# Kernel optimization log

Hardware: AMD Instinct MI355X
Metric: run time of the kernel (lower is better)

Reference implementation:

```python
import jax, jax.numpy as jnp
import numpy as np

# Dimensions (AlphaFold-scale IPA / GeometricFrameAttention)
B, N = 1, 768
C_S, C_Z, C_H, H, PQ, PV = 384, 128, 16, 12, 4, 8
INF = 1e9
EPS = 1e-8
SOFTPLUS_INV_1 = 0.541324854612918  # gfa_point_weights_init_


def quat_to_rot(q):
    """Unit-normalize quaternions [..., 4] -> rotation matrices [..., 3, 3]."""
    q = q / jnp.linalg.norm(q, axis=-1, keepdims=True)
    w, x, y, z = q[..., 0], q[..., 1], q[..., 2], q[..., 3]
    R = jnp.stack([
        1 - 2 * (y * y + z * z), 2 * (x * y - w * z), 2 * (x * z + w * y),
        2 * (x * y + w * z), 1 - 2 * (x * x + z * z), 2 * (y * z - w * x),
        2 * (x * z - w * y), 2 * (y * z + w * x), 1 - 2 * (x * x + y * y),
    ], axis=-1)
    return R.reshape(q.shape[:-1] + (3, 3))


def setup_inputs() -> dict:
    key = jax.random.key(0)
    ks = jax.random.split(key, 12)

    def lin(k, out_d, in_d):
        return jax.random.normal(k, (out_d, in_d), jnp.float32) * (1.0 / np.sqrt(in_d))

    out_in = H * C_H + H * PV * 4 + H * C_Z  # o + o_pt(x,y,z) + o_pt_norm + o_pair
    inp = {
        "s": jax.random.normal(ks[0], (B, N, C_S), jnp.float32),
        "z": jax.random.normal(ks[1], (B, N, N, C_Z), jnp.float32),
        "rot": quat_to_rot(jax.random.normal(ks[2], (B, N, 4), jnp.float32)),
        "trans": jax.random.normal(ks[3], (B, N, 3), jnp.float32),
        "mask": jnp.ones((B, N), jnp.float32),
        "Wq": lin(ks[4], H * C_H, C_S),
        "bq": jnp.zeros((H * C_H,), jnp.float32),
        "Wkv": lin(ks[5], H * 2 * C_H, C_S),
        "bkv": jnp.zeros((H * 2 * C_H,), jnp.float32),
        "Wqp": lin(ks[6], H * PQ * 3, C_S),
        "bqp": jnp.zeros((H * PQ * 3,), jnp.float32),
        "Wkvp": lin(ks[7], H * (PQ + PV) * 3, C_S),
        "bkvp": jnp.zeros((H * (PQ + PV) * 3,), jnp.float32),
        "Wb": lin(ks[8], H, C_Z),
        "bb": jnp.zeros((H,), jnp.float32),
        "head_w": jnp.full((H,), SOFTPLUS_INV_1, jnp.float32),
        "Wout": lin(ks[9], C_S, out_in),
        "bout": jnp.zeros((C_S,), jnp.float32),
    }
    return inp


def _forward(s, z, rot, trans, mask, Wq, bq, Wkv, bkv, Wqp, bqp, Wkvp, bkvp,
             Wb, bb, head_w, Wout, bout):
    Bn, Nn, _ = s.shape
    # scalar q/k/v
    q = (s @ Wq.T + bq).reshape(Bn, Nn, H, C_H)
    kv = (s @ Wkv.T + bkv).reshape(Bn, Nn, H, 2 * C_H)
    k, v = kv[..., :C_H], kv[..., C_H:]
    # point q/k/v: local frame -> global frame (x_glob = R x_loc + t)
    q_pts = (s @ Wqp.T + bqp).reshape(Bn, Nn, H * PQ, 3)
    q_pts = (jnp.einsum('bnxy,bnpy->bnpx', rot, q_pts) + trans[:, :, None]).reshape(Bn, Nn, H, PQ, 3)
    kv_pts = (s @ Wkvp.T + bkvp).reshape(Bn, Nn, H * (PQ + PV), 3)
    kv_pts = (jnp.einsum('bnxy,bnpy->bnpx', rot, kv_pts) + trans[:, :, None]).reshape(Bn, Nn, H, PQ + PV, 3)
    k_pts, v_pts = kv_pts[..., :PQ, :], kv_pts[..., PQ:, :]
    # pair bias [B,N,N,H] -> [B,H,N,N]
    bias = z @ Wb.T + bb
    a = jnp.einsum('bihc,bjhc->bhij', q, k) * np.float32(np.sqrt(1.0 / (3 * C_H)))
    a = a + np.float32(np.sqrt(1.0 / 3.0)) * jnp.transpose(bias, (0, 3, 1, 2))
    # point distance term: sum_p |q_p - k_p|^2 = |q|^2 + |k|^2 - 2 q.k (no [B,N,N,H,P,3] tensor)
    q2 = jnp.sum(q_pts ** 2, axis=(-1, -2))  # [B,N,H]
    k2 = jnp.sum(k_pts ** 2, axis=(-1, -2))
    qk = jnp.einsum('bihpc,bjhpc->bhij', q_pts, k_pts)
    d2 = q2.transpose(0, 2, 1)[..., :, None] + k2.transpose(0, 2, 1)[..., None, :] - 2.0 * qk
    hw = jax.nn.softplus(head_w) * np.float32(np.sqrt(2.0 / (27.0 * PQ)))  # sqrt(1/(3*(PQ*9/2)))
    a = a - 0.5 * hw[None, :, None, None] * d2
    # mask bias
    sq_mask = mask[..., :, None] * mask[..., None, :]
    a = a + (INF * (sq_mask - 1.0))[:, None]
    a = jax.nn.softmax(a, axis=-1)  # [B,H,N,N]
    # outputs
    o = jnp.einsum('bhij,bjhc->bihc', a, v).reshape(Bn, Nn, H * C_H)
    o_pt = jnp.einsum('bhij,bjhpc->bihpc', a, v_pts)  # global frame
    o_pt = jnp.einsum('bnyx,bnhpy->bnhpx', rot, o_pt - trans[:, :, None, None])  # back to local
    o_pt_norm = jnp.sqrt(jnp.sum(o_pt ** 2, axis=-1) + EPS).reshape(Bn, Nn, H * PV)
    o_pt_flat = jnp.moveaxis(o_pt, -1, -3).reshape(Bn, Nn, 3 * H * PV)  # coord-major like unbind+cat
    o_pair = jnp.einsum('bhij,bijc->bihc', a, z).reshape(Bn, Nn, H * C_Z)
    cat = jnp.concatenate([o, o_pt_flat, o_pt_norm, o_pair], axis=-1)
    return cat @ Wout.T + bout


def reference(s, z, rot, trans, mask, Wq, bq, Wkv, bkv, Wqp, bqp, Wkvp, bkvp,
              Wb, bb, head_w, Wout, bout):
    return _forward(s, z, rot, trans, mask, Wq, bq, Wkv, bkv, Wqp, bqp,
                    Wkvp, bkvp, Wb, bb, head_w, Wout, bout)
```

## Files before the change

### kernel.cpp

```cpp
#include <hip/hip_runtime.h>
#include <math.h>

#define NN 768
#define CS 384
#define CZ 128
#define CH 16
#define HH 12
#define PQ 4
#define PV 8
#define OUTIN 2112

#define SC_QK 0.14433756729740643f
#define SC_B  0.57735026918962576f
#define SC_HW 0.13608276348795434f
#define MSLACK 12.0f

__device__ __forceinline__ float dpp_add(float x, const int ctrl) {
    int yi;
    switch (ctrl) {
        case 0: yi = __builtin_amdgcn_update_dpp(0, __float_as_int(x), 0xB1,  0xf, 0xf, true); break;
        case 1: yi = __builtin_amdgcn_update_dpp(0, __float_as_int(x), 0x4E,  0xf, 0xf, true); break;
        case 2: yi = __builtin_amdgcn_update_dpp(0, __float_as_int(x), 0x141, 0xf, 0xf, true); break;
        default:yi = __builtin_amdgcn_update_dpp(0, __float_as_int(x), 0x140, 0xf, 0xf, true); break;
    }
    return x + __int_as_float(yi);
}
__device__ __forceinline__ float dpp_max(float x, const int ctrl) {
    int yi;
    switch (ctrl) {
        case 0: yi = __builtin_amdgcn_update_dpp(0, __float_as_int(x), 0xB1,  0xf, 0xf, true); break;
        case 1: yi = __builtin_amdgcn_update_dpp(0, __float_as_int(x), 0x4E,  0xf, 0xf, true); break;
        case 2: yi = __builtin_amdgcn_update_dpp(0, __float_as_int(x), 0x141, 0xf, 0xf, true); break;
        default:yi = __builtin_amdgcn_update_dpp(0, __float_as_int(x), 0x140, 0xf, 0xf, true); break;
    }
    return fmaxf(x, __int_as_float(yi));
}

__global__ __launch_bounds__(256) void kproj(
    const float* __restrict__ s,
    const float* __restrict__ Wq,  const float* __restrict__ bq,
    const float* __restrict__ Wkv, const float* __restrict__ bkv,
    const float* __restrict__ Wqp, const float* __restrict__ bqp,
    const float* __restrict__ Wkvp,const float* __restrict__ bkvp,
    float* __restrict__ q, float* __restrict__ kT, float* __restrict__ vall,
    float* __restrict__ qpr, float* __restrict__ kvpr)
{
    __shared__ float s_lds[8*384];
    int n0 = blockIdx.x * 8;
    int t = threadIdx.x;
    for (int idx = t; idx < 8*384; idx += 256)
        s_lds[idx] = s[(n0 + idx/384)*384 + (idx%384)];
    __syncthreads();

    int o = blockIdx.y * 128 + (t & 127);
    int ng = t >> 7;
    const float* wrow; float bias;
    if (o < 192)      { wrow = Wq   + o*384;       bias = bq[o]; }
    else if (o < 576) { wrow = Wkv  + (o-192)*384; bias = bkv[o-192]; }
    else if (o < 720) { wrow = Wqp  + (o-576)*384; bias = bqp[o-576]; }
    else              { wrow = Wkvp + (o-720)*384; bias = bkvp[o-720]; }

    float acc[4] = {bias, bias, bias, bias};
    const float4* wr4 = reinterpret_cast<const float4*>(wrow);
    for (int c4 = 0; c4 < 96; ++c4) {
        float4 w = wr4[c4];
        #pragma unroll
        for (int nn = 0; nn < 4; ++nn) {
            const float* sr = &s_lds[(ng*4+nn)*384 + c4*4];
            acc[nn] = fmaf(w.x, sr[0], acc[nn]);
            acc[nn] = fmaf(w.y, sr[1], acc[nn]);
            acc[nn] = fmaf(w.z, sr[2], acc[nn]);
            acc[nn] = fmaf(w.w, sr[3], acc[nn]);
        }
    }
    #pragma unroll
    for (int nn = 0; nn < 4; ++nn) {
        int n = n0 + ng*4 + nn;
        float v = acc[nn];
        if (o < 192)      q[n*192 + o] = v;
        else if (o < 576) {
            int oo = o - 192, h = oo >> 5, cc = oo & 31;
            if (cc < 16) kT[(h*NN + n)*16 + cc] = v;
            else         vall[(size_t)n*480 + h*40 + (cc-16)] = v;
        }
        else if (o < 720) qpr[n*144 + (o-576)] = v;
        else              kvpr[n*432 + (o-720)] = v;
    }
}

__global__ __launch_bounds__(192) void krot(
    const float* __restrict__ rot, const float* __restrict__ trans,
    const float* __restrict__ qpr, const float* __restrict__ kvpr,
    float* __restrict__ qp, float* __restrict__ kpT, float* __restrict__ vall)
{
    int n = blockIdx.x;
    __shared__ float R[9], T[3];
    int t = threadIdx.x;
    if (t < 9) R[t] = rot[n*9 + t];
    if (t < 3) T[t] = trans[n*3 + t];
    __syncthreads();

    const float* src = (t < 48) ? (qpr + n*144 + t*3) : (kvpr + n*432 + (t-48)*3);
    float x = src[0], y = src[1], z = src[2];
    float wx = R[0]*x + R[1]*y + R[2]*z + T[0];
    float wy = R[3]*x + R[4]*y + R[5]*z + T[1];
    float wz = R[6]*x + R[7]*y + R[8]*z + T[2];
    if (t < 48) {
        float* d = qp + n*144 + t*3;
        d[0]=wx; d[1]=wy; d[2]=wz;
    } else {
        int pi = t - 48, h = pi/12, pp = pi%12;
        if (pp < 4) {
            float* d = kpT + (h*NN+n)*12 + pp*3;
            d[0]=wx; d[1]=wy; d[2]=wz;
        } else {
            float* d = vall + (size_t)n*480 + h*40 + 16 + (pp-4)*3;
            d[0]=wx; d[1]=wy; d[2]=wz;
        }
    }
}

__global__ __launch_bounds__(256) void kqk(
    const float* __restrict__ kT, const float* __restrict__ kpT,
    const float* __restrict__ q, const float* __restrict__ qp,
    const float* __restrict__ mask, const float* __restrict__ head_w,
    const float* __restrict__ bb, float* __restrict__ lqd,
    float* __restrict__ mpart)
{
    const int j0 = blockIdx.x * 64;
    const int i0 = blockIdx.y * 32;
    __shared__ float ktl[64][17], kpl[64][13];
    __shared__ float ql[32][17],  qpl[32][13];
    __shared__ float mi_l[32], mj_l[64];
    __shared__ float mpl[32][12];
    const int t = threadIdx.x;
    if (t < 32) mi_l[t] = mask[i0 + t];
    if (t < 64) mj_l[t] = mask[j0 + t];

    const int jl = t & 63, wv = t >> 6;

    for (int h = 0; h < 12; ++h) {
        __syncthreads();
        for (int idx = t; idx < 1024; idx += 256)
            ktl[idx >> 4][idx & 15] = kT[(size_t)(h*NN + j0 + (idx >> 4))*16 + (idx & 15)];
        for (int idx = t; idx < 768; idx += 256) {
            int r = idx / 12, e = idx - r*12;
            kpl[r][e] = kpT[(size_t)(h*NN + j0 + r)*12 + e];
        }
        for (int idx = t; idx < 512; idx += 256)
            ql[idx >> 4][idx & 15] = q[(i0 + (idx >> 4))*192 + h*16 + (idx & 15)];
        for (int idx = t; idx < 384; idx += 256) {
            int r = idx / 12, e = idx - r*12;
            qpl[r][e] = qp[(i0 + r)*144 + h*12 + e];
        }
        __syncthreads();

        const float hwh = log1pf(expf(head_w[h])) * SC_HW;
        const float bbh = bb[h] * SC_B;
        const float mj = mj_l[jl];
        #pragma unroll
        for (int k = 0; k < 8; ++k) {
            const int il = wv*8 + k;
            float qk = 0.f;
            #pragma unroll
            for (int c = 0; c < 16; ++c) qk = fmaf(ktl[jl][c], ql[il][c], qk);
            float d2 = 0.f;
            #pragma unroll
            for (int e = 0; e < 12; ++e) { float d = qpl[il][e] - kpl[jl][e]; d2 = fmaf(d, d, d2); }
            float mt = 1e9f * (mi_l[il]*mj - 1.0f);
            float lg = fmaf(qk, SC_QK, fmaf(-0.5f*hwh, d2, bbh)) + mt;
            lqd[((size_t)(i0+il)*NN + j0 + jl)*12 + h] = lg;
            float m = lg;
            m = dpp_max(m, 0);
            m = dpp_max(m, 1);
            m = dpp_max(m, 2);
            m = dpp_max(m, 3);
            m = fmaxf(m, __shfl_xor(m, 16, 64));
            m = fmaxf(m, __shfl_xor(m, 32, 64));
            if (jl == 0) mpl[il][h] = m;
        }
    }
    __syncthreads();
    if (t < 384) {
        int il = t / 12, h = t - il*12;
        mpart[((size_t)h*NN + i0 + il)*12 + blockIdx.x] = mpl[il][h];
    }
}

__global__ __launch_bounds__(256) void kfuse(
    const float* __restrict__ z, const float* __restrict__ Wb,
    const float* __restrict__ lqd, const float* __restrict__ mpart,
    const float* __restrict__ vall,
    float* __restrict__ opart, float* __restrict__ vpart, float* __restrict__ ssum)
{
    __shared__ float  M_lds[12];
    __shared__ __align__(16) float p_lds[12][68];
    __shared__ __align__(16) float p_T[64][16];
    __shared__ float2 ofold[4][12][64];
    __shared__ float  sredL[16][6];

    const int i = blockIdx.x, jseg = blockIdx.y;
    const int t = threadIdx.x, w = t >> 6, l = t & 63;
    const int gid = t >> 4, cl = t & 15;
    const int hhalf = gid & 1, h0 = hhalf * 6, jofs = gid >> 1;

    if (t < 12) {
        const float4* mp = (const float4*)(mpart + ((size_t)t*NN + i)*12);
        float4 a = mp[0], b = mp[1], c = mp[2];
        float m = fmaxf(fmaxf(fmaxf(a.x,a.y), fmaxf(a.z,a.w)),
                 fmaxf(fmaxf(fmaxf(b.x,b.y), fmaxf(b.z,b.w)),
                       fmaxf(fmaxf(c.x,c.y), fmaxf(c.z,c.w))));
        M_lds[t] = m + MSLACK;
    }

    float4 wva[6], wvb[6];
    #pragma unroll
    for (int h = 0; h < 6; ++h) {
        const float4* wp = (const float4*)(Wb + (h0+h)*CZ + cl*8);
        wva[h] = wp[0]; wvb[h] = wp[1];
    }

    float2 oa[12];
    #pragma unroll
    for (int h = 0; h < 12; ++h) { oa[h].x = 0.f; oa[h].y = 0.f; }
    float2 vacc; vacc.x = 0.f; vacc.y = 0.f;
    const int vch = 2*t;
    const int vh  = (t < 240) ? (vch / 40) : 0;
    float s_acc = 0.f;

    __syncthreads();
    const float Mh = M_lds[h0 + (cl < 6 ? cl : 5)];
    const int jbase = jseg * 192;

    for (int tile = 0; tile < 3; ++tile) {
        const int jt = jbase + tile*64;

        {
            const float4* zq0 = (const float4*)(z + ((size_t)i*NN + jt + jofs)*CZ) + cl*2;
            float4 za = zq0[0], zb = zq0[1];
            for (int it = 0; it < 8; ++it) {
                float4 zaN = za, zbN = zb;
                if (it + 1 < 8) {
                    const float4* zq = (const float4*)(z + ((size_t)i*NN + jt + (it+1)*8 + jofs)*CZ) + cl*2;
                    zaN = zq[0]; zbN = zq[1];
                }
                const int j = jt + it*8 + jofs;
                float b0, b1, b2, b3, b4, b5;
                #define BDOT(BV, H)                                \
                    BV = za.x*wva[H].x;                            \
                    BV = fmaf(za.y, wva[H].y, BV);                 \
                    BV = fmaf(za.z, wva[H].z, BV);                 \
                    BV = fmaf(za.w, wva[H].w, BV);                 \
                    BV = fmaf(zb.x, wvb[H].x, BV);                 \
                    BV = fmaf(zb.y, wvb[H].y, BV);                 \
                    BV = fmaf(zb.z, wvb[H].z, BV);                 \
                    BV = fmaf(zb.w, wvb[H].w, BV);
                BDOT(b0, 0) BDOT(b1, 1) BDOT(b2, 2) BDOT(b3, 3) BDOT(b4, 4) BDOT(b5, 5)
                #undef BDOT
                #define BRED(BV)                                   \
                    BV = dpp_add(BV, 0);                           \
                    BV = dpp_add(BV, 1);                           \
                    BV = dpp_add(BV, 2);                           \
                    BV = dpp_add(BV, 3);
                BRED(b0) BRED(b1) BRED(b2) BRED(b3) BRED(b4) BRED(b5)
                #undef BRED
                float bsel = b0;
                bsel = (cl == 1) ? b1 : bsel;
                bsel = (cl == 2) ? b2 : bsel;
                bsel = (cl == 3) ? b3 : bsel;
                bsel = (cl == 4) ? b4 : bsel;
                bsel = (cl == 5) ? b5 : bsel;
                if (cl < 6) {
                    float g = fmaf(bsel, SC_B, lqd[((size_t)i*NN + j)*12 + h0 + cl]);
                    float p = __expf(g - Mh);
                    p_lds[h0 + cl][j - jt] = p;
                    p_T[j - jt][h0 + cl] = p;
                    s_acc += p;
                }
                za = zaN; zb = zbN;
            }
        }
        __syncthreads();

        {
            const float2* zr2 = (const float2*)(z + (size_t)i*NN*CZ) + l;
            #pragma unroll 4
            for (int jj = 0; jj < 16; ++jj) {
                const int jb = jj*4 + w;
                float2 zv = zr2[(size_t)(jt + jb)*64];
                float4 pA = *(const float4*)&p_T[jb][0];
                float4 pB = *(const float4*)&p_T[jb][4];
                float4 pC = *(const float4*)&p_T[jb][8];
                oa[0].x  = fmaf(pA.x, zv.x, oa[0].x);  oa[0].y  = fmaf(pA.x, zv.y, oa[0].y);
                oa[1].x  = fmaf(pA.y, zv.x, oa[1].x);  oa[1].y  = fmaf(pA.y, zv.y, oa[1].y);
                oa[2].x  = fmaf(pA.z, zv.x, oa[2].x);  oa[2].y  = fmaf(pA.z, zv.y, oa[2].y);
                oa[3].x  = fmaf(pA.w, zv.x, oa[3].x);  oa[3].y  = fmaf(pA.w, zv.y, oa[3].y);
                oa[4].x  = fmaf(pB.x, zv.x, oa[4].x);  oa[4].y  = fmaf(pB.x, zv.y, oa[4].y);
                oa[5].x  = fmaf(pB.y, zv.x, oa[5].x);  oa[5].y  = fmaf(pB.y, zv.y, oa[5].y);
                oa[6].x  = fmaf(pB.z, zv.x, oa[6].x);  oa[6].y  = fmaf(pB.z, zv.y, oa[6].y);
                oa[7].x  = fmaf(pB.w, zv.x, oa[7].x);  oa[7].y  = fmaf(pB.w, zv.y, oa[7].y);
                oa[8].x  = fmaf(pC.x, zv.x, oa[8].x);  oa[8].y  = fmaf(pC.x, zv.y, oa[8].y);
                oa[9].x  = fmaf(pC.y, zv.x, oa[9].x);  oa[9].y  = fmaf(pC.y, zv.y, oa[9].y);
                oa[10].x = fmaf(pC.z, zv.x, oa[10].x); oa[10].y = fmaf(pC.z, zv.y, oa[10].y);
                oa[11].x = fmaf(pC.w, zv.x, oa[11].x); oa[11].y = fmaf(pC.w, zv.y, oa[11].y);
            }
        }

        if (t < 240) {
            const float2* vr = (const float2*)(vall + (size_t)jt*480 + vch);
            #pragma unroll 4
            for (int q4 = 0; q4 < 16; ++q4) {
                float4 pv = *(const float4*)&p_lds[vh][q4*4];
                float2 v0 = vr[(size_t)(q4*4+0)*240];
                float2 v1 = vr[(size_t)(q4*4+1)*240];
                float2 v2 = vr[(size_t)(q4*4+2)*240];
                float2 v3 = vr[(size_t)(q4*4+3)*240];
                vacc.x = fmaf(pv.x, v0.x, vacc.x); vacc.y = fmaf(pv.x, v0.y, vacc.y);
                vacc.x = fmaf(pv.y, v1.x, vacc.x); vacc.y = fmaf(pv.y, v1.y, vacc.y);
                vacc.x = fmaf(pv.z, v2.x, vacc.x); vacc.y = fmaf(pv.z, v2.y, vacc.y);
                vacc.x = fmaf(pv.w, v3.x, vacc.x); vacc.y = fmaf(pv.w, v3.y, vacc.y);
            }
        }
        __syncthreads();
    }

    #pragma unroll
    for (int h = 0; h < 12; ++h) ofold[w][h][l] = oa[h];
    if (cl < 6) sredL[gid][cl] = s_acc;
    if (t < 240)
        *((float2*)(vpart + ((size_t)(jseg*NN + i))*480) + t) = vacc;
    __syncthreads();

    float2* opw = (float2*)(opart + ((size_t)(jseg*NN + i))*1536);
    #pragma unroll
    for (int k = 0; k < 3; ++k) {
        int slot = k*256 + t;
        int h = slot >> 6, c2 = slot & 63;
        float2 v0 = ofold[0][h][c2], v1 = ofold[1][h][c2];
        float2 v2 = ofold[2][h][c2], v3 = ofold[3][h][c2];
        float2 o;
        o.x = v0.x + v1.x + v2.x + v3.x;
        o.y = v0.y + v1.y + v2.y + v3.y;
        opw[slot] = o;
    }
    if (t < 12) {
        float sv = 0.f;
        #pragma unroll
        for (int k = 0; k < 8; ++k) sv += sredL[k*2 + (t/6)][t % 6];
        ssum[(size_t)(jseg*12 + t)*NN + i] = sv;
    }
}

__global__ __launch_bounds__(256) void kepi(
    const float* __restrict__ opart, const float* __restrict__ vpart,
    const float* __restrict__ ssum, const float* __restrict__ rot,
    const float* __restrict__ trans, float* __restrict__ cat)
{
    __shared__ float sinv[12];
    __shared__ float optl[12][24];
    __shared__ float R[9], T[3];
    const int i = blockIdx.x, t = threadIdx.x;
    if (t < 9) R[t] = rot[i*9 + t];
    if (t < 3) T[t] = trans[i*3 + t];
    if (t >= 16 && t < 28) {
        int h = t - 16;
        sinv[h] = 1.0f / (ssum[(size_t)h*NN + i] + ssum[(size_t)(12+h)*NN + i]
                        + ssum[(size_t)(24+h)*NN + i] + ssum[(size_t)(36+h)*NN + i]);
    }
    __syncthreads();

    float* crow = cat + (size_t)i*OUTIN;
    const float2* op0 = (const float2*)(opart + (size_t)i*1536);
    const float2* op1 = (const float2*)(opart + (size_t)(NN + i)*1536);
    const float2* op2 = (const float2*)(opart + (size_t)(2*NN + i)*1536);
    const float2* op3 = (const float2*)(opart + (size_t)(3*NN + i)*1536);
    #pragma unroll
    for (int k = 0; k < 3; ++k) {
        int slot = k*256 + t;
        int h = slot >> 6, c2 = slot & 63;
        float2 a = op0[slot], b = op1[slot], c = op2[slot], d = op3[slot];
        float sc = sinv[h];
        float2 o;
        o.x = (a.x + b.x + c.x + d.x)*sc;
        o.y = (a.y + b.y + c.y + d.y)*sc;
        *(float2*)(crow + 576 + h*128 + c2*2) = o;
    }
    if (t < 240) {
        const int ch = 2*t, h = ch/40, e = ch%40;
        float2 v0 = *(const float2*)(vpart + (size_t)i*480 + ch);
        float2 v1 = *(const float2*)(vpart + (size_t)(NN + i)*480 + ch);
        float2 v2 = *(const float2*)(vpart + (size_t)(2*NN + i)*480 + ch);
        float2 v3 = *(const float2*)(vpart + (size_t)(3*NN + i)*480 + ch);
        float sc = sinv[h];
        float vx = (v0.x + v1.x + v2.x + v3.x)*sc;
        float vy = (v0.y + v1.y + v2.y + v3.y)*sc;
        if (e < 16) { crow[h*16 + e] = vx; crow[h*16 + e + 1] = vy; }
        else        { optl[h][e-16] = vx; optl[h][e-15] = vy; }
    }
    __syncthreads();
    if (t < 96) {
        int h = t >> 3, pp = t & 7;
        float wx = optl[h][pp*3+0] - T[0];
        float wy = optl[h][pp*3+1] - T[1];
        float wz = optl[h][pp*3+2] - T[2];
        crow[192 + 0*96 + h*8 + pp] = R[0]*wx + R[3]*wy + R[6]*wz;
        crow[192 + 1*96 + h*8 + pp] = R[1]*wx + R[4]*wy + R[7]*wz;
        crow[192 + 2*96 + h*8 + pp] = R[2]*wx + R[5]*wy + R[8]*wz;
        crow[480 + h*8 + pp] = sqrtf(fmaf(wx,wx,fmaf(wy,wy,wz*wz)) + 1e-8f);
    }
}

__global__ __launch_bounds__(256) void koutp(
    const float* __restrict__ cat, const float* __restrict__ Wout,
    float* __restrict__ ptmp)
{
    __shared__ float ct[32][36];
    __shared__ float wt[64][36];
    const int n0 = blockIdx.x * 32, o0 = blockIdx.y * 64;
    const int k0 = blockIdx.z * 352;
    const int t = threadIdx.x;
    const int tn = (t >> 4) * 2;
    const int to = t & 15;

    float a00=0,a01=0,a02=0,a03=0, a10=0,a11=0,a12=0,a13=0;

    for (int c = 0; c < 11; ++c) {
        __syncthreads();
        #pragma unroll
        for (int u = 0; u < 4; ++u) {
            int idx = u*256 + t, r = idx >> 5, cc = idx & 31;
            ct[r][cc] = cat[(size_t)(n0 + r)*OUTIN + k0 + c*32 + cc];
        }
        #pragma unroll
        for (int u = 0; u < 8; ++u) {
            int idx = u*256 + t, r = idx >> 5, cc = idx & 31;
            wt[r][cc] = Wout[(size_t)(o0 + r)*OUTIN + k0 + c*32 + cc];
        }
        __syncthreads();
        #pragma unroll
        for (int kk = 0; kk < 32; kk += 4) {
            float4 c0 = *(const float4*)&ct[tn][kk];
            float4 c1 = *(const float4*)&ct[tn+1][kk];
            float4 w0 = *(const float4*)&wt[to][kk];
            float4 w1 = *(const float4*)&wt[to+16][kk];
            float4 w2 = *(const float4*)&wt[to+32][kk];
            float4 w3 = *(const float4*)&wt[to+48][kk];
            a00 = fmaf(c0.x,w0.x,a00); a00 = fmaf(c0.y,w0.y,a00); a00 = fmaf(c0.z,w0.z,a00); a00 = fmaf(c0.w,w0.w,a00);
            a01 = fmaf(c0.x,w1.x,a01); a01 = fmaf(c0.y,w1.y,a01); a01 = fmaf(c0.z,w1.z,a01); a01 = fmaf(c0.w,w1.w,a01);
            a02 = fmaf(c0.x,w2.x,a02); a02 = fmaf(c0.y,w2.y,a02); a02 = fmaf(c0.z,w2.z,a02); a02 = fmaf(c0.w,w2.w,a02);
            a03 = fmaf(c0.x,w3.x,a03); a03 = fmaf(c0.y,w3.y,a03); a03 = fmaf(c0.z,w3.z,a03); a03 = fmaf(c0.w,w3.w,a03);
            a10 = fmaf(c1.x,w0.x,a10); a10 = fmaf(c1.y,w0.y,a10); a10 = fmaf(c1.z,w0.z,a10); a10 = fmaf(c1.w,w0.w,a10);
            a11 = fmaf(c1.x,w1.x,a11); a11 = fmaf(c1.y,w1.y,a11); a11 = fmaf(c1.z,w1.z,a11); a11 = fmaf(c1.w,w1.w,a11);
            a12 = fmaf(c1.x,w2.x,a12); a12 = fmaf(c1.y,w2.y,a12); a12 = fmaf(c1.z,w2.z,a12); a12 = fmaf(c1.w,w2.w,a12);
            a13 = fmaf(c1.x,w3.x,a13); a13 = fmaf(c1.y,w3.y,a13); a13 = fmaf(c1.z,w3.z,a13); a13 = fmaf(c1.w,w3.w,a13);
        }
    }
    float* pb = ptmp + (size_t)blockIdx.z * (NN*384);
    pb[(size_t)(n0+tn+0)*384 + o0+to+ 0] = a00;
    pb[(size_t)(n0+tn+0)*384 + o0+to+16] = a01;
    pb[(size_t)(n0+tn+0)*384 + o0+to+32] = a02;
    pb[(size_t)(n0+tn+0)*384 + o0+to+48] = a03;
    pb[(size_t)(n0+tn+1)*384 + o0+to+ 0] = a10;
    pb[(size_t)(n0+tn+1)*384 + o0+to+16] = a11;
    pb[(size_t)(n0+tn+1)*384 + o0+to+32] = a12;
    pb[(size_t)(n0+tn+1)*384 + o0+to+48] = a13;
}

__global__ __launch_bounds__(256) void kred(
    const float* __restrict__ ptmp, const float* __restrict__ bout,
    float* __restrict__ out)
{
    int idx = blockIdx.x * 256 + threadIdx.x;
    int o = idx % 384;
    float v = bout[o];
    #pragma unroll
    for (int s = 0; s < 6; ++s) v += ptmp[(size_t)s*(NN*384) + idx];
    out[idx] = v;
}

extern "C" void kernel_launch(void* const* d_in, const int* in_sizes, int n_in,
                              void* d_out, int out_size, void* d_ws, size_t ws_size,
                              hipStream_t stream) {
    const float* s      = (const float*)d_in[0];
    const float* z      = (const float*)d_in[1];
    const float* rot    = (const float*)d_in[2];
    const float* trans  = (const float*)d_in[3];
    const float* mask   = (const float*)d_in[4];
    const float* Wq     = (const float*)d_in[5];
    const float* bq     = (const float*)d_in[6];
    const float* Wkv    = (const float*)d_in[7];
    const float* bkv    = (const float*)d_in[8];
    const float* Wqp    = (const float*)d_in[9];
    const float* bqp    = (const float*)d_in[10];
    const float* Wkvp   = (const float*)d_in[11];
    const float* bkvp   = (const float*)d_in[12];
    const float* Wb     = (const float*)d_in[13];
    const float* bb     = (const float*)d_in[14];
    const float* head_w = (const float*)d_in[15];
    const float* Wout   = (const float*)d_in[16];
    const float* bout   = (const float*)d_in[17];
    float* out = (float*)d_out;
    float* ws  = (float*)d_ws;

    float* vall  = ws;
    float* mpart = ws + 368640;
    float* ssum  = ws + 479232;
    float* cat   = ws + 516096;
    float* lqd   = ws + 2138112;
    float* opart = ws + 9216000;
    float* vpart = ws + 13934592;
    float* q     = ws + 15409152;
    float* kT    = ws + 15556608;
    float* kpT   = ws + 15704064;
    float* qp    = ws + 15814656;
    float* qpr   = ws + 15925248;
    float* kvpr  = ws + 16035840;
    float* ptmp  = lqd;

    kproj<<<dim3(96, 9), 256, 0, stream>>>(s, Wq, bq, Wkv, bkv, Wqp, bqp, Wkvp, bkvp,
                                           q, kT, vall, qpr, kvpr);
    krot<<<dim3(768), 192, 0, stream>>>(rot, trans, qpr, kvpr, qp, kpT, vall);
    kqk<<<dim3(12, 24), 256, 0, stream>>>(kT, kpT, q, qp, mask, head_w, bb, lqd, mpart);
    kfuse<<<dim3(768, 4), 256, 0, stream>>>(z, Wb, lqd, mpart, vall, opart, vpart, ssum);
    kepi<<<dim3(768), 256, 0, stream>>>(opart, vpart, ssum, rot, trans, cat);
    koutp<<<dim3(24, 6, 6), 256, 0, stream>>>(cat, Wout, ptmp);
    kred<<<dim3(1152), 256, 0, stream>>>(ptmp, bout, out);
}
```

Measured before the change: 411.2 us.

## Fuse pair-output accumulation into bias pass to reuse loaded z tiles

The kfuse kernel no longer re-reads z from global memory in a second pass for the attention-weighted pair output. Instead, each thread computes all six head probabilities for its row j and accumulates p*z directly into 48 register accumulators, using the z values already loaded for the bias dot product. The transposed p_T buffer is dropped, and the final cross-group reduction becomes an 8-step serialized LDS accumulation. This halves z traffic but raises register pressure and adds six exp evaluations per thread plus more syncthreads in the epilogue.

```diff
diff --git a/kernel.cpp b/kernel.cpp
--- a/kernel.cpp
+++ b/kernel.cpp
@@ -195,12 +195,11 @@
 {
     __shared__ float  M_lds[12];
     __shared__ __align__(16) float p_lds[12][68];
-    __shared__ __align__(16) float p_T[64][16];
-    __shared__ float2 ofold[4][12][64];
+    __shared__ __align__(16) float oacc[12][128];
     __shared__ float  sredL[16][6];
 
     const int i = blockIdx.x, jseg = blockIdx.y;
-    const int t = threadIdx.x, w = t >> 6, l = t & 63;
+    const int t = threadIdx.x;
     const int gid = t >> 4, cl = t & 15;
     const int hhalf = gid & 1, h0 = hhalf * 6, jofs = gid >> 1;
 
@@ -220,16 +219,21 @@
         wva[h] = wp[0]; wvb[h] = wp[1];
     }
 
-    float2 oa[12];
+    float4 oaA[6], oaB[6];
     #pragma unroll
-    for (int h = 0; h < 12; ++h) { oa[h].x = 0.f; oa[h].y = 0.f; }
+    for (int h = 0; h < 6; ++h) {
+        oaA[h].x = 0.f; oaA[h].y = 0.f; oaA[h].z = 0.f; oaA[h].w = 0.f;
+        oaB[h].x = 0.f; oaB[h].y = 0.f; oaB[h].z = 0.f; oaB[h].w = 0.f;
+    }
+
     float2 vacc; vacc.x = 0.f; vacc.y = 0.f;
     const int vch = 2*t;
     const int vh  = (t < 240) ? (vch / 40) : 0;
     float s_acc = 0.f;
 
     __syncthreads();
-    const float Mh = M_lds[h0 + (cl < 6 ? cl : 5)];
+    const float M0 = M_lds[h0+0], M1 = M_lds[h0+1], M2 = M_lds[h0+2];
+    const float M3 = M_lds[h0+3], M4 = M_lds[h0+4], M5 = M_lds[h0+5];
     const int jbase = jseg * 192;
 
     for (int tile = 0; tile < 3; ++tile) {
@@ -264,47 +268,43 @@
                     BV = dpp_add(BV, 3);
                 BRED(b0) BRED(b1) BRED(b2) BRED(b3) BRED(b4) BRED(b5)
                 #undef BRED
-                float bsel = b0;
-                bsel = (cl == 1) ? b1 : bsel;
-                bsel = (cl == 2) ? b2 : bsel;
-                bsel = (cl == 3) ? b3 : bsel;
-                bsel = (cl == 4) ? b4 : bsel;
-                bsel = (cl == 5) ? b5 : bsel;
+                const float* lq = lqd + ((size_t)i*NN + j)*12 + h0;
+                float2 q01 = *(const float2*)(lq + 0);
+                float2 q23 = *(const float2*)(lq + 2);
+                float2 q45 = *(const float2*)(lq + 4);
+                float p0 = __expf(fmaf(b0, SC_B, q01.x) - M0);
+                float p1 = __expf(fmaf(b1, SC_B, q01.y) - M1);
+                float p2 = __expf(fmaf(b2, SC_B, q23.x) - M2);
+                float p3 = __expf(fmaf(b3, SC_B, q23.y) - M3);
+                float p4 = __expf(fmaf(b4, SC_B, q45.x) - M4);
+                float p5 = __expf(fmaf(b5, SC_B, q45.y) - M5);
+
+                #define OACC(K, PV)                                              \
+                    oaA[K].x = fmaf(PV, za.x, oaA[K].x);                         \
+                    oaA[K].y = fmaf(PV, za.y, oaA[K].y);                         \
+                    oaA[K].z = fmaf(PV, za.z, oaA[K].z);                         \
+                    oaA[K].w = fmaf(PV, za.w, oaA[K].w);                         \
+                    oaB[K].x = fmaf(PV, zb.x, oaB[K].x);                         \
+                    oaB[K].y = fmaf(PV, zb.y, oaB[K].y);                         \
+                    oaB[K].z = fmaf(PV, zb.z, oaB[K].z);                         \
+                    oaB[K].w = fmaf(PV, zb.w, oaB[K].w);
+                OACC(0, p0) OACC(1, p1) OACC(2, p2) OACC(3, p3) OACC(4, p4) OACC(5, p5)
+                #undef OACC
+
+                float ps = p0;
+                ps = (cl == 1) ? p1 : ps;
+                ps = (cl == 2) ? p2 : ps;
+                ps = (cl == 3) ? p3 : ps;
+                ps = (cl == 4) ? p4 : ps;
+                ps = (cl == 5) ? p5 : ps;
                 if (cl < 6) {
-                    float g = fmaf(bsel, SC_B, lqd[((size_t)i*NN + j)*12 + h0 + cl]);
-                    float p = __expf(g - Mh);
-                    p_lds[h0 + cl][j - jt] = p;
-                    p_T[j - jt][h0 + cl] = p;
-                    s_acc += p;
+                    p_lds[h0 + cl][j - jt] = ps;
+                    s_acc += ps;
                 }
                 za = zaN; zb = zbN;
             }
         }
         __syncthreads();
-
-        {
-            const float2* zr2 = (const float2*)(z + (size_t)i*NN*CZ) + l;
-            #pragma unroll 4
-            for (int jj = 0; jj < 16; ++jj) {
-                const int jb = jj*4 + w;
-                float2 zv = zr2[(size_t)(jt + jb)*64];
-                float4 pA = *(const float4*)&p_T[jb][0];
-                float4 pB = *(const float4*)&p_T[jb][4];
-                float4 pC = *(const float4*)&p_T[jb][8];
-                oa[0].x  = fmaf(pA.x, zv.x, oa[0].x);  oa[0].y  = fmaf(pA.x, zv.y, oa[0].y);
-                oa[1].x  = fmaf(pA.y, zv.x, oa[1].x);  oa[1].y  = fmaf(pA.y, zv.y, oa[1].y);
-                oa[2].x  = fmaf(pA.z, zv.x, oa[2].x);  oa[2].y  = fmaf(pA.z, zv.y, oa[2].y);
-                oa[3].x  = fmaf(pA.w, zv.x, oa[3].x);  oa[3].y  = fmaf(pA.w, zv.y, oa[3].y);
-                oa[4].x  = fmaf(pB.x, zv.x, oa[4].x);  oa[4].y  = fmaf(pB.x, zv.y, oa[4].y);
-                oa[5].x  = fmaf(pB.y, zv.x, oa[5].x);  oa[5].y  = fmaf(pB.y, zv.y, oa[5].y);
-                oa[6].x  = fmaf(pB.z, zv.x, oa[6].x);  oa[6].y  = fmaf(pB.z, zv.y, oa[6].y);
-                oa[7].x  = fmaf(pB.w, zv.x, oa[7].x);  oa[7].y  = fmaf(pB.w, zv.y, oa[7].y);
-                oa[8].x  = fmaf(pC.x, zv.x, oa[8].x);  oa[8].y  = fmaf(pC.x, zv.y, oa[8].y);
-                oa[9].x  = fmaf(pC.y, zv.x, oa[9].x);  oa[9].y  = fmaf(pC.y, zv.y, oa[9].y);
-                oa[10].x = fmaf(pC.z, zv.x, oa[10].x); oa[10].y = fmaf(pC.z, zv.y, oa[10].y);
-                oa[11].x = fmaf(pC.w, zv.x, oa[11].x); oa[11].y = fmaf(pC.w, zv.y, oa[11].y);
-            }
-        }
 
         if (t < 240) {
             const float2* vr = (const float2*)(vall + (size_t)jt*480 + vch);
@@ -324,24 +324,36 @@
         __syncthreads();
     }
 
-    #pragma unroll
-    for (int h = 0; h < 12; ++h) ofold[w][h][l] = oa[h];
     if (cl < 6) sredL[gid][cl] = s_acc;
     if (t < 240)
         *((float2*)(vpart + ((size_t)(jseg*NN + i))*480) + t) = vacc;
-    __syncthreads();
-
-    float2* opw = (float2*)(opart + ((size_t)(jseg*NN + i))*1536);
-    #pragma unroll
-    for (int k = 0; k < 3; ++k) {
-        int slot = k*256 + t;
-        int h = slot >> 6, c2 = slot & 63;
-        float2 v0 = ofold[0][h][c2], v1 = ofold[1][h][c2];
-        float2 v2 = ofold[2][h][c2], v3 = ofold[3][h][c2];
-        float2 o;
-        o.x = v0.x + v1.x + v2.x + v3.x;
-        o.y = v0.y + v1.y + v2.y + v3.y;
-        opw[slot] = o;
+
+    for (int g = 0; g < 8; ++g) {
+        if (jofs == g) {
+            #pragma unroll
+            for (int k = 0; k < 6; ++k) {
+                float4* pa = (float4*)&oacc[h0+k][cl*8];
+                float4* pb = (float4*)&oacc[h0+k][cl*8+4];
+                if (g == 0) {
+                    pa[0] = oaA[k];
+                    pb[0] = oaB[k];
+                } else {
+                    float4 a = pa[0], b = pb[0];
+                    a.x += oaA[k].x; a.y += oaA[k].y; a.z += oaA[k].z; a.w += oaA[k].w;
+                    b.x += oaB[k].x; b.y += oaB[k].y; b.z += oaB[k].z; b.w += oaB[k].w;
+                    pa[0] = a;
+                    pb[0] = b;
+                }
+            }
+        }
+        __syncthreads();
+    }
+
+    {
+        float* opw = opart + ((size_t)(jseg*NN + i))*1536;
+        const float* of = &oacc[0][0];
+        #pragma unroll
+        for (int k = 0; k < 6; ++k) opw[k*256 + t] = of[k*256 + t];
     }
     if (t < 12) {
         float sv = 0.f;
```

Measured after the change: 394.0 us. 4.2% less time.
